# Performance work log

Hardware: AMD Instinct MI355X
Metric: run time of the kernel (lower is better)

Reference implementation:

```python
import jax, jax.numpy as jnp
import numpy as np


def setup_inputs() -> dict:
    key = jax.random.key(0)
    k_x, k_w1, k_w2 = jax.random.split(key, 3)
    b, d, m, h = 256, 2048, 64, 128  # batch, d_model, history_length, d_out
    lim1 = 1.0 / np.sqrt(m + h)
    lim2 = 1.0 / np.sqrt(h + d)
    x = jax.random.normal(k_x, (b, d, m), dtype=jnp.float32)
    w1 = jax.random.uniform(k_w1, (m, h, d), dtype=jnp.float32, minval=-lim1, maxval=lim1)
    b1 = jnp.zeros((1, h, d), dtype=jnp.float32)
    w2 = jax.random.uniform(k_w2, (h, d), dtype=jnp.float32, minval=-lim2, maxval=lim2)
    b2 = jnp.zeros((1, h), dtype=jnp.float32)
    return {"x": x, "w1": w1, "b1": b1, "w2": w2, "b2": b2}


def reference(x, w1, b1, w2, b2):
    # per-neuron (per-d) MLP: contract over history m, then over hidden h
    hidden = jnp.einsum('bdm,mhd->bhd', x, w1) + b1  # (b, h, d)
    out = jnp.einsum('bhd,hd->bh', hidden, w2) + b2  # (b, h)
    return out
```

## Files before the change

kernel.cpp:

```cpp
#include <hip/hip_runtime.h>

typedef unsigned short u16;
typedef __attribute__((ext_vector_type(8))) short short8;
typedef __attribute__((ext_vector_type(4))) float f32x4;

#define D_TOT 2048
#define M_TOT 64
#define H_TOT 128
#define B_TOT 256
#define NG    256
#define XB    131072
#define W1M   262144

__device__ __forceinline__ u16 f2bf(float f) {
  unsigned u = __builtin_bit_cast(unsigned, f);
  u = (u + 0x7fffu + ((u >> 16) & 1u)) >> 16;
  return (u16)u;
}
__device__ __forceinline__ float bf2f(u16 v) {
  unsigned u = ((unsigned)v) << 16;
  return __builtin_bit_cast(float, u);
}

__global__ __launch_bounds__(256)
void nlm_pw(const float* __restrict__ w1, const float* __restrict__ w2,
            const float* __restrict__ b1, const float* __restrict__ b2,
            u16* __restrict__ Bp, float* __restrict__ ch) {
  __shared__ __align__(16) u16 tile[32 * 8 * 64];
  const int t = threadIdx.x;

  if (blockIdx.x >= 1024) {
    const int h = blockIdx.x - 1024;
    const float4* pb = (const float4*)(b1 + (size_t)h * D_TOT);
    const float4* pw = (const float4*)(w2 + (size_t)h * D_TOT);
    float s = 0.f;
    for (int i = t; i < D_TOT / 4; i += 256) {
      float4 a = pb[i], w = pw[i];
      s += a.x * w.x + a.y * w.y + a.z * w.z + a.w * w.w;
    }
    float* red = (float*)tile;
    red[t] = s;
    __syncthreads();
    for (int off = 128; off > 0; off >>= 1) {
      if (t < off) red[t] += red[t + off];
      __syncthreads();
    }
    if (t == 0) ch[h] = red[0] + b2[h];
    return;
  }

  const int gq  = blockIdx.x & 63;
  const int hb  = blockIdx.x >> 6;
  const int dq0 = gq * 32;

#pragma unroll
  for (int rep = 0; rep < 2; ++rep) {
    const int tau = rep * 256 + t;
    const int h_l = tau >> 6, m = tau & 63;
    const int h   = hb * 8 + h_l;
    const float* w1p = w1 + (size_t)m * W1M + (size_t)h * D_TOT + dq0;
    const float* w2p = w2 + (size_t)h * D_TOT + dq0;
    u16* dst = tile + h_l * 64 + m;
#pragma unroll
    for (int q = 0; q < 8; ++q) {
      float4 a = *(const float4*)(w1p + q * 4);
      float4 s = *(const float4*)(w2p + q * 4);
      dst[(q * 4 + 0) * 512] = f2bf(a.x * s.x);
      dst[(q * 4 + 1) * 512] = f2bf(a.y * s.y);
      dst[(q * 4 + 2) * 512] = f2bf(a.z * s.z);
      dst[(q * 4 + 3) * 512] = f2bf(a.w * s.w);
    }
  }
  __syncthreads();
#pragma unroll 4
  for (int dc = 0; dc < 32; ++dc) {
    const int g = gq * 4 + (dc >> 3), c = dc & 7;
    u16* out = Bp + (((size_t)g * 8 + c) * H_TOT + hb * 8) * 64 + t * 2;
    *(ushort2*)out = *(const ushort2*)(tile + dc * 512 + t * 2);
  }
}

__global__ __launch_bounds__(512, 4)
void nlm_p1(const float* __restrict__ x, const u16* __restrict__ Bp,
            u16* __restrict__ partial) {
  __shared__ __align__(16) u16 As[64 * 72];
  __shared__ __align__(16) u16 Bs[128 * 72];

  const int tid  = threadIdx.x;
  const int g    = blockIdx.x & 255;
  const int bq   = blockIdx.x >> 8;
  const int d0   = g * 8;
  const int lane = tid & 63, wave = tid >> 6;
  const int wm   = wave >> 2;
  const int wn   = wave & 3;
  const int quad = lane >> 4, l16 = lane & 15;

  const int a_bl = tid >> 3, a_p = tid & 7;
  const float* xrow = x + (size_t)(bq * 64 + a_bl) * XB
                        + (size_t)d0 * M_TOT + a_p * 8;
  const int b_h = tid >> 2, b_qp = tid & 3;
  const u16* bsrc = Bp + ((size_t)g * 8 * H_TOT + b_h) * 64 + b_qp * 16;

  f32x4 acc[2][2];
#pragma unroll
  for (int i = 0; i < 2; ++i)
#pragma unroll
    for (int j = 0; j < 2; ++j) acc[i][j] = (f32x4){0.f, 0.f, 0.f, 0.f};

  float4 v0  = *(const float4*)(xrow);
  float4 v1  = *(const float4*)(xrow + 4);
  short8 bv0 = *(const short8*)(bsrc);
  short8 bv1 = *(const short8*)(bsrc + 8);

#pragma unroll
  for (int c = 0; c < 8; ++c) {
    {
      short8 av;
      av[0] = (short)f2bf(v0.x); av[1] = (short)f2bf(v0.y);
      av[2] = (short)f2bf(v0.z); av[3] = (short)f2bf(v0.w);
      av[4] = (short)f2bf(v1.x); av[5] = (short)f2bf(v1.y);
      av[6] = (short)f2bf(v1.z); av[7] = (short)f2bf(v1.w);
      *(short8*)(As + a_bl * 72 + a_p * 8) = av;
      *(short8*)(Bs + b_h * 72 + b_qp * 16)     = bv0;
      *(short8*)(Bs + b_h * 72 + b_qp * 16 + 8) = bv1;
    }
    __syncthreads();
    if (c < 7) {
      const float* xp = xrow + (c + 1) * M_TOT;
      v0 = *(const float4*)(xp);
      v1 = *(const float4*)(xp + 4);
      const u16* bp = bsrc + (size_t)(c + 1) * (H_TOT * 64);
      bv0 = *(const short8*)(bp);
      bv1 = *(const short8*)(bp + 8);
    }
#pragma unroll
    for (int s = 0; s < 2; ++s) {
      short8 af[2], bfr[2];
#pragma unroll
      for (int i = 0; i < 2; ++i)
        af[i] = *(const short8*)(As + (wm * 32 + i * 16 + l16) * 72 + s * 32 + quad * 8);
#pragma unroll
      for (int j = 0; j < 2; ++j)
        bfr[j] = *(const short8*)(Bs + (wn * 32 + j * 16 + l16) * 72 + s * 32 + quad * 8);
#pragma unroll
      for (int i = 0; i < 2; ++i)
#pragma unroll
        for (int j = 0; j < 2; ++j)
          acc[i][j] = __builtin_amdgcn_mfma_f32_16x16x32_bf16(af[i], bfr[j], acc[i][j], 0, 0, 0);
    }
    __syncthreads();
  }

#pragma unroll
  for (int i = 0; i < 2; ++i)
#pragma unroll
    for (int j = 0; j < 2; ++j) {
      const int hcol = wn * 32 + j * 16 + l16;
#pragma unroll
      for (int r = 0; r < 4; ++r) {
        const int brow = bq * 64 + wm * 32 + i * 16 + quad * 4 + r;
        partial[((size_t)brow * NG + g) * H_TOT + hcol] = f2bf(acc[i][j][r]);
      }
    }
}

__global__ __launch_bounds__(256)
void nlm_p2(const u16* __restrict__ partial, const float* __restrict__ ch,
            float* __restrict__ out) {
  const int b = blockIdx.x, t = threadIdx.x;
  const int h2   = t & 63;
  const int half = t >> 6;
  const u16* base = partial + ((size_t)b * NG + half * 64) * H_TOT + 2 * h2;
  float s0 = 0.f, s1 = 0.f;
#pragma unroll 8
  for (int gg = 0; gg < 64; ++gg) {
    unsigned v = __builtin_nontemporal_load((const unsigned*)(base + (size_t)gg * H_TOT));
    s0 += bf2f((u16)(v & 0xffffu));
    s1 += bf2f((u16)(v >> 16));
  }
  __shared__ float red0[256], red1[256];
  red0[t] = s0;
  red1[t] = s1;
  __syncthreads();
  if (t < 64) {
    float a0 = red0[t] + red0[t + 64] + red0[t + 128] + red0[t + 192];
    float a1 = red1[t] + red1[t + 64] + red1[t + 128] + red1[t + 192];
    out[(size_t)b * H_TOT + 2 * t]     = a0 + ch[2 * t];
    out[(size_t)b * H_TOT + 2 * t + 1] = a1 + ch[2 * t + 1];
  }
}

extern "C" void kernel_launch(void* const* d_in, const int* in_sizes, int n_in,
                              void* d_out, int out_size, void* d_ws, size_t ws_size,
                              hipStream_t stream) {
  const float* x  = (const float*)d_in[0];
  const float* w1 = (const float*)d_in[1];
  const float* b1 = (const float*)d_in[2];
  const float* w2 = (const float*)d_in[3];
  const float* b2 = (const float*)d_in[4];
  float* out = (float*)d_out;

  u16*   partial = (u16*)d_ws;
  u16*   Bp      = (u16*)((char*)d_ws + (size_t)B_TOT * NG * H_TOT * sizeof(u16));
  float* ch      = (float*)((char*)d_ws + (size_t)B_TOT * NG * H_TOT * sizeof(u16)
                                        + (size_t)NG * 8 * H_TOT * 64 * sizeof(u16));

  nlm_pw<<<dim3(1152), dim3(256), 0, stream>>>(w1, w2, b1, b2, Bp, ch);
  nlm_p1<<<dim3(1024), dim3(512), 0, stream>>>(x, Bp, partial);
  nlm_p2<<<dim3(256),  dim3(256), 0, stream>>>(partial, ch, out);
}
```

Measured before the change: 262.2 us.

## Double batch tile per block and double-buffer global prefetch in GEMM stage

Each p1 block now covers 128 batch rows instead of 64, so every B tile loaded from global memory is reused across twice as many rows and the grid is halved to 512 blocks. Global loads are prefetched two chunks ahead into two register sets, and __syncthreads is replaced by an explicit LDS waitcnt plus s_barrier. Each wave now computes a 32x64 output tile (8 accumulators), which raises register pressure and leaves fewer blocks to spread across the CUs.

```diff
diff --git a/kernel.cpp b/kernel.cpp
--- a/kernel.cpp
+++ b/kernel.cpp
@@ -20,6 +20,14 @@
 __device__ __forceinline__ float bf2f(u16 v) {
   unsigned u = ((unsigned)v) << 16;
   return __builtin_bit_cast(float, u);
+}
+__device__ __forceinline__ short8 pack8(float4 a, float4 b) {
+  short8 t;
+  t[0] = (short)f2bf(a.x); t[1] = (short)f2bf(a.y);
+  t[2] = (short)f2bf(a.z); t[3] = (short)f2bf(a.w);
+  t[4] = (short)f2bf(b.x); t[5] = (short)f2bf(b.y);
+  t[6] = (short)f2bf(b.z); t[7] = (short)f2bf(b.w);
+  return t;
 }
 
 __global__ __launch_bounds__(256)
@@ -83,7 +91,7 @@
 __global__ __launch_bounds__(512, 4)
 void nlm_p1(const float* __restrict__ x, const u16* __restrict__ Bp,
             u16* __restrict__ partial) {
-  __shared__ __align__(16) u16 As[64 * 72];
+  __shared__ __align__(16) u16 As[128 * 72];
   __shared__ __align__(16) u16 Bs[128 * 72];
 
   const int tid  = threadIdx.x;
@@ -91,74 +99,95 @@
   const int bq   = blockIdx.x >> 8;
   const int d0   = g * 8;
   const int lane = tid & 63, wave = tid >> 6;
-  const int wm   = wave >> 2;
-  const int wn   = wave & 3;
+  const int wm   = wave & 3;
+  const int wn   = wave >> 2;
   const int quad = lane >> 4, l16 = lane & 15;
 
-  const int a_bl = tid >> 3, a_p = tid & 7;
-  const float* xrow = x + (size_t)(bq * 64 + a_bl) * XB
-                        + (size_t)d0 * M_TOT + a_p * 8;
+  const int a_bl = tid >> 2, a_p = tid & 3;
+  const float* xrow = x + (size_t)(bq * 128 + a_bl) * XB
+                        + (size_t)d0 * M_TOT + a_p * 16;
   const int b_h = tid >> 2, b_qp = tid & 3;
   const u16* bsrc = Bp + ((size_t)g * 8 * H_TOT + b_h) * 64 + b_qp * 16;
 
-  f32x4 acc[2][2];
+  f32x4 acc[2][4];
 #pragma unroll
   for (int i = 0; i < 2; ++i)
 #pragma unroll
-    for (int j = 0; j < 2; ++j) acc[i][j] = (f32x4){0.f, 0.f, 0.f, 0.f};
-
-  float4 v0  = *(const float4*)(xrow);
-  float4 v1  = *(const float4*)(xrow + 4);
-  short8 bv0 = *(const short8*)(bsrc);
-  short8 bv1 = *(const short8*)(bsrc + 8);
+    for (int j = 0; j < 4; ++j) acc[i][j] = (f32x4){0.f, 0.f, 0.f, 0.f};
+
+  float4 A0q0, A0q1, A0q2, A0q3;  short8 B0v0, B0v1;
+  float4 A1q0, A1q1, A1q2, A1q3;  short8 B1v0, B1v1;
+
+  {
+    const float* p = xrow;
+    A0q0 = *(const float4*)(p);      A0q1 = *(const float4*)(p + 4);
+    A0q2 = *(const float4*)(p + 8);  A0q3 = *(const float4*)(p + 12);
+    B0v0 = *(const short8*)(bsrc);   B0v1 = *(const short8*)(bsrc + 8);
+    const float* q = xrow + 1 * M_TOT;
+    A1q0 = *(const float4*)(q);      A1q1 = *(const float4*)(q + 4);
+    A1q2 = *(const float4*)(q + 8);  A1q3 = *(const float4*)(q + 12);
+    const u16* bp = bsrc + (size_t)1 * (H_TOT * 64);
+    B1v0 = *(const short8*)(bp);     B1v1 = *(const short8*)(bp + 8);
+  }
 
 #pragma unroll
   for (int c = 0; c < 8; ++c) {
     {
-      short8 av;
-      av[0] = (short)f2bf(v0.x); av[1] = (short)f2bf(v0.y);
-      av[2] = (short)f2bf(v0.z); av[3] = (short)f2bf(v0.w);
-      av[4] = (short)f2bf(v1.x); av[5] = (short)f2bf(v1.y);
-      av[6] = (short)f2bf(v1.z); av[7] = (short)f2bf(v1.w);
-      *(short8*)(As + a_bl * 72 + a_p * 8) = av;
-      *(short8*)(Bs + b_h * 72 + b_qp * 16)     = bv0;
-      *(short8*)(Bs + b_h * 72 + b_qp * 16 + 8) = bv1;
-    }
-    __syncthreads();
-    if (c < 7) {
-      const float* xp = xrow + (c + 1) * M_TOT;
-      v0 = *(const float4*)(xp);
-      v1 = *(const float4*)(xp + 4);
-      const u16* bp = bsrc + (size_t)(c + 1) * (H_TOT * 64);
-      bv0 = *(const short8*)(bp);
-      bv1 = *(const short8*)(bp + 8);
-    }
+      float4 q0 = (c & 1) ? A1q0 : A0q0;
+      float4 q1 = (c & 1) ? A1q1 : A0q1;
+      float4 q2 = (c & 1) ? A1q2 : A0q2;
+      float4 q3 = (c & 1) ? A1q3 : A0q3;
+      short8 v0 = (c & 1) ? B1v0 : B0v0;
+      short8 v1 = (c & 1) ? B1v1 : B0v1;
+      *(short8*)(As + a_bl * 72 + a_p * 16)     = pack8(q0, q1);
+      *(short8*)(As + a_bl * 72 + a_p * 16 + 8) = pack8(q2, q3);
+      *(short8*)(Bs + b_h * 72 + b_qp * 16)     = v0;
+      *(short8*)(Bs + b_h * 72 + b_qp * 16 + 8) = v1;
+    }
+    asm volatile("s_waitcnt lgkmcnt(0)" ::: "memory");
+    __builtin_amdgcn_s_barrier();
+
+    if (c + 2 < 8) {
+      const float* p = xrow + (c + 2) * M_TOT;
+      const u16*  bp = bsrc + (size_t)(c + 2) * (H_TOT * 64);
+      if ((c & 1) == 0) {
+        A0q0 = *(const float4*)(p);      A0q1 = *(const float4*)(p + 4);
+        A0q2 = *(const float4*)(p + 8);  A0q3 = *(const float4*)(p + 12);
+        B0v0 = *(const short8*)(bp);     B0v1 = *(const short8*)(bp + 8);
+      } else {
+        A1q0 = *(const float4*)(p);      A1q1 = *(const float4*)(p + 4);
+        A1q2 = *(const float4*)(p + 8);  A1q3 = *(const float4*)(p + 12);
+        B1v0 = *(const short8*)(bp);     B1v1 = *(const short8*)(bp + 8);
+      }
+    }
+
 #pragma unroll
     for (int s = 0; s < 2; ++s) {
-      short8 af[2], bfr[2];
+      short8 af[2], bfr[4];
 #pragma unroll
       for (int i = 0; i < 2; ++i)
         af[i] = *(const short8*)(As + (wm * 32 + i * 16 + l16) * 72 + s * 32 + quad * 8);
 #pragma unroll
-      for (int j = 0; j < 2; ++j)
-        bfr[j] = *(const short8*)(Bs + (wn * 32 + j * 16 + l16) * 72 + s * 32 + quad * 8);
+      for (int j = 0; j < 4; ++j)
+        bfr[j] = *(const short8*)(Bs + (wn * 64 + j * 16 + l16) * 72 + s * 32 + quad * 8);
 #pragma unroll
       for (int i = 0; i < 2; ++i)
 #pragma unroll
-        for (int j = 0; j < 2; ++j)
+        for (int j = 0; j < 4; ++j)
           acc[i][j] = __builtin_amdgcn_mfma_f32_16x16x32_bf16(af[i], bfr[j], acc[i][j], 0, 0, 0);
     }
-    __syncthreads();
+    asm volatile("s_waitcnt lgkmcnt(0)" ::: "memory");
+    __builtin_amdgcn_s_barrier();
   }
 
 #pragma unroll
   for (int i = 0; i < 2; ++i)
 #pragma unroll
-    for (int j = 0; j < 2; ++j) {
-      const int hcol = wn * 32 + j * 16 + l16;
+    for (int j = 0; j < 4; ++j) {
+      const int hcol = wn * 64 + j * 16 + l16;
 #pragma unroll
       for (int r = 0; r < 4; ++r) {
-        const int brow = bq * 64 + wm * 32 + i * 16 + quad * 4 + r;
+        const int brow = bq * 128 + wm * 32 + i * 16 + quad * 4 + r;
         partial[((size_t)brow * NG + g) * H_TOT + hcol] = f2bf(acc[i][j][r]);
       }
     }
@@ -206,6 +235,6 @@
                                         + (size_t)NG * 8 * H_TOT * 64 * sizeof(u16));
 
   nlm_pw<<<dim3(1152), dim3(256), 0, stream>>>(w1, w2, b1, b2, Bp, ch);
-  nlm_p1<<<dim3(1024), dim3(512), 0, stream>>>(x, Bp, partial);
+  nlm_p1<<<dim3(512),  dim3(512), 0, stream>>>(x, Bp, partial);
   nlm_p2<<<dim3(256),  dim3(256), 0, stream>>>(partial, ch, out);
 }
```

New measurement: 262.0 us. Within noise of the previous version (-0.1%).
